# Kernel optimization log

Measured on AMD Instinct MI355X. Metric: run time of the kernel, lower is better.

## Reference

```python
import jax, jax.numpy as jnp
import numpy as np

# dims: B=batch, N1=in_channels (primary caps), P=pcap_n_dims, N2=n_caps, D=n_dims
B, N1, P, N2, D = 64, 1152, 8, 128, 16
ROUTINGS = 2


def squash(s, axis=-1):
    # squash_factor * unit_vector, with eps-stabilized norm (matches torch.finfo eps)
    sq_norm = jnp.sum(s * s, axis=axis, keepdims=True)
    norm = jnp.sqrt(sq_norm + jnp.finfo(s.dtype).eps)
    return (sq_norm / (1.0 + sq_norm)) * (s / norm)


def setup_inputs() -> dict:
    key = jax.random.key(0)
    k1, k2 = jax.random.split(key)
    x = jax.random.normal(k1, (B, N1, P), dtype=jnp.float32)
    # learned transform W: nn.Parameter(torch.randn(1, N1, N2, D, P)); leading 1 dropped
    W = jax.random.normal(k2, (N1, N2, D, P), dtype=jnp.float32)
    return {"x": x, "W": W}


def reference(x, W):
    b, n1 = x.shape[0], x.shape[1]
    n2 = W.shape[1]
    # caps2_predicted[b,i,n,d] = sum_p W[i,n,d,p] * x[b,i,p]  (the tiled batched matmul)
    pred = jnp.einsum('indp,bip->bind', W, x)  # [B, N1, N2, D]
    raw = jnp.zeros((b, n1, n2), dtype=pred.dtype)  # routing logits
    v = None
    for i in range(ROUTINGS):
        c = jax.nn.softmax(raw, axis=2)                  # softmax over output capsules
        s = jnp.einsum('bin,bind->bnd', c, pred)         # weighted sum over input caps
        v = squash(s, axis=-1)                           # [B, N2, D]
        if i < ROUTINGS - 1:
            # agreement: <prediction, output> over the D dimension
            raw = raw + jnp.einsum('bind,bnd->bin', pred, v)
    return v  # [B, n_caps, n_dims]
```

## Files before the change

### kernel.cpp

```cpp
#include <hip/hip_runtime.h>
#include <math.h>

#define B_   64
#define P_   8
#define N1_  1152
#define N2_  128
#define D_   16

#define NSPLIT 32
#define CHUNK  (N1_ / NSPLIT)
#define NIB    (CHUNK / 4)

typedef __attribute__((ext_vector_type(8)))  short bf16x8;
typedef __attribute__((ext_vector_type(4)))  float f32x4;
typedef __attribute__((ext_vector_type(16))) float f32x16;

__device__ inline void split_frag(float4 a0, float4 a1, bf16x8& hi, bf16x8& lo)
{
    float w[8] = {a0.x, a0.y, a0.z, a0.w, a1.x, a1.y, a1.z, a1.w};
#pragma unroll
    for (int j = 0; j < 8; ++j) {
        unsigned ub = __float_as_uint(w[j]);
        hi[j] = (short)(ub >> 16);
        float hif = __uint_as_float(ub & 0xffff0000u);
        float r = w[j] - hif;
        lo[j] = (short)(__float_as_uint(r) >> 16);
    }
}

__device__ inline void split_arr(const float* w, bf16x8& hi, bf16x8& lo)
{
#pragma unroll
    for (int j = 0; j < 8; ++j) {
        unsigned ub = __float_as_uint(w[j]);
        hi[j] = (short)(ub >> 16);
        float hif = __uint_as_float(ub & 0xffff0000u);
        float r = w[j] - hif;
        lo[j] = (short)(__float_as_uint(r) >> 16);
    }
}

__device__ inline void split4_pack(float4 s, uint2& hp, uint2& lp)
{
    float w[4] = {s.x, s.y, s.z, s.w};
    unsigned hs[4], ls[4];
#pragma unroll
    for (int j = 0; j < 4; ++j) {
        unsigned ub = __float_as_uint(w[j]);
        hs[j] = ub >> 16;
        float hif = __uint_as_float(ub & 0xffff0000u);
        float r = w[j] - hif;
        ls[j] = __float_as_uint(r) >> 16;
    }
    hp.x = hs[0] | (hs[1] << 16); hp.y = hs[2] | (hs[3] << 16);
    lp.x = ls[0] | (ls[1] << 16); lp.y = ls[2] | (ls[3] << 16);
}

__global__ __launch_bounds__(128) void k0_xt(const float* __restrict__ x,
                                             float* __restrict__ xt,
                                             unsigned short* __restrict__ xth,
                                             unsigned short* __restrict__ xtl,
                                             float* __restrict__ denom)
{
    const int i  = blockIdx.x;
    const int t  = threadIdx.x;
    const int b  = t >> 1, ph = t & 1;
    float4 v = *(const float4*)(x + ((size_t)b * N1_ + i) * P_ + ph * 4);
    const size_t off = (size_t)i * (64 * P_) + b * P_ + ph * 4;
    *(float4*)(xt + off) = v;
    uint2 hp, lp;
    split4_pack(v, hp, lp);
    *(uint2*)(xth + off) = hp;
    *(uint2*)(xtl + off) = lp;
    int z = i * 128 + t;
    if (z < N1_ * 64) denom[z] = 0.f;
}

__global__ __launch_bounds__(256) void k1_s0_mfma(const unsigned short* __restrict__ xth,
                                                  const unsigned short* __restrict__ xtl,
                                                  const float* __restrict__ W,
                                                  float* __restrict__ s0p)
{
    const int tid   = threadIdx.x;
    const int lane  = tid & 63;
    const int wv    = tid >> 6;
    const int col   = lane & 15;
    const int quad  = lane >> 4;
    const int b     = wv * 16 + col;
    const int nbase = blockIdx.x * 4;
    const int isp   = blockIdx.y;
    const int ibase = isp * CHUNK;

    f32x4 acc[4];
#pragma unroll
    for (int nn = 0; nn < 4; ++nn) acc[nn] = (f32x4){0.f, 0.f, 0.f, 0.f};

    const unsigned short* xh = xth + (size_t)(ibase + quad) * (64 * P_) + b * P_;
    const unsigned short* xl = xtl + (size_t)(ibase + quad) * (64 * P_) + b * P_;

    for (int ib = 0; ib < NIB; ++ib) {
        const int i0 = ibase + ib * 4;
        bf16x8 bhi = *(const bf16x8*)xh;
        bf16x8 blo = *(const bf16x8*)xl;
        xh += 4 * 64 * P_;
        xl += 4 * 64 * P_;
#pragma unroll
        for (int nn = 0; nn < 4; ++nn) {
            const float* wp = W + (((size_t)(i0 + quad) * N2_ + nbase + nn) * D_ + col) * P_;
            float4 wa = *(const float4*)wp;
            float4 wb = *(const float4*)(wp + 4);
            bf16x8 ahi, alo;
            split_frag(wa, wb, ahi, alo);
            acc[nn] = __builtin_amdgcn_mfma_f32_16x16x32_bf16(ahi, bhi, acc[nn], 0, 0, 0);
            acc[nn] = __builtin_amdgcn_mfma_f32_16x16x32_bf16(ahi, blo, acc[nn], 0, 0, 0);
            acc[nn] = __builtin_amdgcn_mfma_f32_16x16x32_bf16(alo, bhi, acc[nn], 0, 0, 0);
        }
    }
#pragma unroll
    for (int nn = 0; nn < 4; ++nn) {
        float4 v = make_float4(acc[nn][0], acc[nn][1], acc[nn][2], acc[nn][3]);
        *(float4*)(s0p + (size_t)isp * (B_ * N2_ * D_) + (size_t)b * (N2_ * D_)
                   + (nbase + nn) * D_ + quad * 4) = v;
    }
}

__global__ __launch_bounds__(256) void k2_squash(const float* __restrict__ spart,
                                                 float* __restrict__ vout,
                                                 unsigned short* __restrict__ v0h,
                                                 unsigned short* __restrict__ v0l,
                                                 float scale, int nsplit)
{
    int idx = blockIdx.x * 256 + threadIdx.x;
    float4 s = make_float4(0.f, 0.f, 0.f, 0.f);
    for (int sp = 0; sp < nsplit; ++sp) {
        float4 t = *(const float4*)(spart + (size_t)sp * (B_ * N2_ * D_) + (size_t)idx * 4);
        s.x += t.x; s.y += t.y; s.z += t.z; s.w += t.w;
    }
    s.x *= scale; s.y *= scale; s.z *= scale; s.w *= scale;
    float sq = s.x * s.x + s.y * s.y + s.z * s.z + s.w * s.w;
    sq += __shfl_xor(sq, 1);
    sq += __shfl_xor(sq, 2);
    float norm = sqrtf(sq + 1.1920929e-7f);
    float f = (sq / (1.f + sq)) / norm;
    float4 o = make_float4(s.x * f, s.y * f, s.z * f, s.w * f);
    *(float4*)(vout + (size_t)idx * 4) = o;
    if (v0h) {
        uint2 hp, lp;
        split4_pack(o, hp, lp);
        *(uint2*)(v0h + (size_t)idx * 4) = hp;
        *(uint2*)(v0l + (size_t)idx * 4) = lp;
    }
}

__global__ __launch_bounds__(256) void k3a2_mfma32(const float* __restrict__ xt,
                                                   const float* __restrict__ W,
                                                   const unsigned short* __restrict__ v0h,
                                                   const unsigned short* __restrict__ v0l,
                                                   float* __restrict__ e_t,
                                                   float* __restrict__ denom)
{
    const int tid  = threadIdx.x;
    const int lane = tid & 63;
    const int wv   = tid >> 6;
    const int m    = lane & 31;
    const int kh   = lane >> 5;
    const int isub = m >> 3;
    const int p    = m & 7;
    const int i0   = blockIdx.y * 4;
    const int nbase = blockIdx.x * 32 + wv * 8;

    float4 xq0[4], xq1[4];
#pragma unroll
    for (int is = 0; is < 4; ++is) {
        const float* xp = xt + (size_t)(i0 + is) * (64 * P_) + m * 8 + kh * 4;
        xq0[is] = *(const float4*)xp;
        xq1[is] = *(const float4*)(xp + 256);
    }

    float dacc[4] = {0.f, 0.f, 0.f, 0.f};

#pragma unroll 1
    for (int nt = 0; nt < 8; ++nt) {
        const int n = nbase + nt;

        bf16x8 vhi[2], vlo[2];
#pragma unroll
        for (int bt = 0; bt < 2; ++bt) {
            const size_t vo = (size_t)(bt * 32 + m) * (N2_ * D_) + n * D_ + kh * 8;
            vhi[bt] = *(const bf16x8*)(v0h + vo);
            vlo[bt] = *(const bf16x8*)(v0l + vo);
        }

        const float* wp = W + ((size_t)(i0 + isub) * N2_ + n) * (D_ * P_) + kh * 64 + p;
        float a[8];
#pragma unroll
        for (int j = 0; j < 8; ++j) a[j] = wp[8 * j];
        bf16x8 ahi, alo;
        split_arr(a, ahi, alo);

        f32x16 acc0, acc1;
#pragma unroll
        for (int r = 0; r < 16; ++r) { acc0[r] = 0.f; acc1[r] = 0.f; }
        acc0 = __builtin_amdgcn_mfma_f32_32x32x16_bf16(ahi, vhi[0], acc0, 0, 0, 0);
        acc0 = __builtin_amdgcn_mfma_f32_32x32x16_bf16(ahi, vlo[0], acc0, 0, 0, 0);
        acc0 = __builtin_amdgcn_mfma_f32_32x32x16_bf16(alo, vhi[0], acc0, 0, 0, 0);
        acc1 = __builtin_amdgcn_mfma_f32_32x32x16_bf16(ahi, vhi[1], acc1, 0, 0, 0);
        acc1 = __builtin_amdgcn_mfma_f32_32x32x16_bf16(ahi, vlo[1], acc1, 0, 0, 0);
        acc1 = __builtin_amdgcn_mfma_f32_32x32x16_bf16(alo, vhi[1], acc1, 0, 0, 0);

#pragma unroll
        for (int is = 0; is < 4; ++is) {
            float r0 = acc0[4 * is] * xq0[is].x + acc0[4 * is + 1] * xq0[is].y
                     + acc0[4 * is + 2] * xq0[is].z + acc0[4 * is + 3] * xq0[is].w;
            float r1 = acc1[4 * is] * xq1[is].x + acc1[4 * is + 1] * xq1[is].y
                     + acc1[4 * is + 2] * xq1[is].z + acc1[4 * is + 3] * xq1[is].w;
            r0 += __shfl_xor(r0, 32);
            r1 += __shfl_xor(r1, 32);
            float e = __expf(kh ? r1 : r0);
            e_t[(size_t)(i0 + is) * (N2_ * 64) + n * 64 + kh * 32 + m] = e;
            dacc[is] += e;
        }
    }

    __shared__ float dred[4][4][64];
#pragma unroll
    for (int is = 0; is < 4; ++is) dred[wv][is][kh * 32 + m] = dacc[is];
    __syncthreads();
    {
        const int is = tid >> 6;
        const int b  = tid & 63;
        float s = dred[0][is][b] + dred[1][is][b] + dred[2][is][b] + dred[3][is][b];
        atomicAdd(&denom[(size_t)(i0 + is) * 64 + b], s);
    }
}

__global__ __launch_bounds__(256) void k3c_s1_mfma(const float* __restrict__ xt,
                                                   const float* __restrict__ W,
                                                   const float* __restrict__ e_t,
                                                   const float* __restrict__ denom,
                                                   float* __restrict__ s1p)
{
    const int tid   = threadIdx.x;
    const int lane  = tid & 63;
    const int wv    = tid >> 6;
    const int col   = lane & 15;
    const int quad  = lane >> 4;
    const int n     = blockIdx.x * 4 + wv;
    const int isp   = blockIdx.y;
    const int ibase = isp * CHUNK;

    f32x4 acc[4];
#pragma unroll
    for (int bt = 0; bt < 4; ++bt) acc[bt] = (f32x4){0.f, 0.f, 0.f, 0.f};

    for (int ib = 0; ib < NIB; ++ib) {
        const int iq = ibase + ib * 4 + quad;
        const float* wp = W + ((size_t)iq * N2_ + n) * (D_ * P_) + col * P_;
        float4 wa = *(const float4*)wp;
        float4 wb = *(const float4*)(wp + 4);
        bf16x8 ahi, alo;
        split_frag(wa, wb, ahi, alo);
#pragma unroll
        for (int bt = 0; bt < 4; ++bt) {
            const int b = bt * 16 + col;
            const float* xp = xt + (size_t)iq * (64 * P_) + b * P_;
            float4 xa = *(const float4*)xp;
            float4 xb = *(const float4*)(xp + 4);
            float e  = e_t[((size_t)iq * N2_ + n) * 64 + b];
            float dv = denom[(size_t)iq * 64 + b];
            float c  = e * __builtin_amdgcn_rcpf(dv);
            float4 ya = make_float4(xa.x * c, xa.y * c, xa.z * c, xa.w * c);
            float4 yb = make_float4(xb.x * c, xb.y * c, xb.z * c, xb.w * c);
            bf16x8 bhi, blo;
            split_frag(ya, yb, bhi, blo);
            acc[bt] = __builtin_amdgcn_mfma_f32_16x16x32_bf16(ahi, bhi, acc[bt], 0, 0, 0);
            acc[bt] = __builtin_amdgcn_mfma_f32_16x16x32_bf16(ahi, blo, acc[bt], 0, 0, 0);
            acc[bt] = __builtin_amdgcn_mfma_f32_16x16x32_bf16(alo, bhi, acc[bt], 0, 0, 0);
        }
    }
#pragma unroll
    for (int bt = 0; bt < 4; ++bt) {
        const int b = bt * 16 + col;
        float4 v = make_float4(acc[bt][0], acc[bt][1], acc[bt][2], acc[bt][3]);
        *(float4*)(s1p + (size_t)isp * (B_ * N2_ * D_) + (size_t)b * (N2_ * D_)
                   + n * D_ + quad * 4) = v;
    }
}

extern "C" void kernel_launch(void* const* d_in, const int* in_sizes, int n_in,
                              void* d_out, int out_size, void* d_ws, size_t ws_size,
                              hipStream_t stream)
{
    const float* x = (const float*)d_in[0];
    const float* W = (const float*)d_in[1];
    float* out = (float*)d_out;

    float* s_part = (float*)d_ws;
    float* v0     = s_part + (size_t)NSPLIT * B_ * N2_ * D_;
    float* e_t    = v0 + B_ * N2_ * D_;
    float* xt     = e_t + (size_t)N1_ * N2_ * 64;
    float* denom  = xt + (size_t)N1_ * 64 * P_;
    unsigned short* xth = (unsigned short*)(denom + (size_t)N1_ * 64);
    unsigned short* xtl = xth + (size_t)N1_ * 64 * P_;
    unsigned short* v0h = xtl + (size_t)N1_ * 64 * P_;
    unsigned short* v0l = v0h + (size_t)B_ * N2_ * D_;

    k0_xt       <<<N1_,               128, 0, stream>>>(x, xt, xth, xtl, denom);
    k1_s0_mfma  <<<dim3(32, NSPLIT),  256, 0, stream>>>(xth, xtl, W, s_part);
    k2_squash   <<<128,               256, 0, stream>>>(s_part, v0, v0h, v0l, 1.f / 128.f, NSPLIT);
    k3a2_mfma32 <<<dim3(4, N1_ / 4),  256, 0, stream>>>(xt, W, v0h, v0l, e_t, denom);
    k3c_s1_mfma <<<dim3(32, NSPLIT),  256, 0, stream>>>(xt, W, e_t, denom, s_part);
    k2_squash   <<<128,               256, 0, stream>>>(s_part, out, nullptr, nullptr, 1.f, NSPLIT);
}
```

Measured before the change: 200.9 us.

## Remap s0 MFMA kernel so each wave owns one capsule across all batches

The first-routing-pass kernel now assigns each wave one output capsule n and loops over four batch tiles. Before, each wave covered one batch tile and four capsules, so the four waves of a block loaded and split the same W fragments four times. Now each W fragment is loaded and split into bf16 hi/lo once per wave, and the small x fragments are reloaded per batch tile instead. The split count over input capsules drops from 32 to 16, which halves the partial-sum buffer the squash kernel must reduce but also halves grid parallelism.

```diff
diff --git a/kernel.cpp b/kernel.cpp
--- a/kernel.cpp
+++ b/kernel.cpp
@@ -7,7 +7,7 @@
 #define N2_  128
 #define D_   16
 
-#define NSPLIT 32
+#define NSPLIT 16
 #define CHUNK  (N1_ / NSPLIT)
 #define NIB    (CHUNK / 4)
 
@@ -86,41 +86,38 @@
     const int wv    = tid >> 6;
     const int col   = lane & 15;
     const int quad  = lane >> 4;
-    const int b     = wv * 16 + col;
-    const int nbase = blockIdx.x * 4;
+    const int n     = blockIdx.x * 4 + wv;
     const int isp   = blockIdx.y;
     const int ibase = isp * CHUNK;
 
     f32x4 acc[4];
 #pragma unroll
-    for (int nn = 0; nn < 4; ++nn) acc[nn] = (f32x4){0.f, 0.f, 0.f, 0.f};
-
-    const unsigned short* xh = xth + (size_t)(ibase + quad) * (64 * P_) + b * P_;
-    const unsigned short* xl = xtl + (size_t)(ibase + quad) * (64 * P_) + b * P_;
+    for (int bt = 0; bt < 4; ++bt) acc[bt] = (f32x4){0.f, 0.f, 0.f, 0.f};
 
     for (int ib = 0; ib < NIB; ++ib) {
-        const int i0 = ibase + ib * 4;
-        bf16x8 bhi = *(const bf16x8*)xh;
-        bf16x8 blo = *(const bf16x8*)xl;
-        xh += 4 * 64 * P_;
-        xl += 4 * 64 * P_;
-#pragma unroll
-        for (int nn = 0; nn < 4; ++nn) {
-            const float* wp = W + (((size_t)(i0 + quad) * N2_ + nbase + nn) * D_ + col) * P_;
-            float4 wa = *(const float4*)wp;
-            float4 wb = *(const float4*)(wp + 4);
-            bf16x8 ahi, alo;
-            split_frag(wa, wb, ahi, alo);
-            acc[nn] = __builtin_amdgcn_mfma_f32_16x16x32_bf16(ahi, bhi, acc[nn], 0, 0, 0);
-            acc[nn] = __builtin_amdgcn_mfma_f32_16x16x32_bf16(ahi, blo, acc[nn], 0, 0, 0);
-            acc[nn] = __builtin_amdgcn_mfma_f32_16x16x32_bf16(alo, bhi, acc[nn], 0, 0, 0);
+        const int iq = ibase + ib * 4 + quad;
+        const float* wp = W + ((size_t)iq * N2_ + n) * (D_ * P_) + col * P_;
+        float4 wa = *(const float4*)wp;
+        float4 wb = *(const float4*)(wp + 4);
+        bf16x8 ahi, alo;
+        split_frag(wa, wb, ahi, alo);
+#pragma unroll
+        for (int bt = 0; bt < 4; ++bt) {
+            const int b = bt * 16 + col;
+            const size_t xo = (size_t)iq * (64 * P_) + b * P_;
+            bf16x8 bhi = *(const bf16x8*)(xth + xo);
+            bf16x8 blo = *(const bf16x8*)(xtl + xo);
+            acc[bt] = __builtin_amdgcn_mfma_f32_16x16x32_bf16(ahi, bhi, acc[bt], 0, 0, 0);
+            acc[bt] = __builtin_amdgcn_mfma_f32_16x16x32_bf16(ahi, blo, acc[bt], 0, 0, 0);
+            acc[bt] = __builtin_amdgcn_mfma_f32_16x16x32_bf16(alo, bhi, acc[bt], 0, 0, 0);
         }
     }
 #pragma unroll
-    for (int nn = 0; nn < 4; ++nn) {
-        float4 v = make_float4(acc[nn][0], acc[nn][1], acc[nn][2], acc[nn][3]);
+    for (int bt = 0; bt < 4; ++bt) {
+        const int b = bt * 16 + col;
+        float4 v = make_float4(acc[bt][0], acc[bt][1], acc[bt][2], acc[bt][3]);
         *(float4*)(s0p + (size_t)isp * (B_ * N2_ * D_) + (size_t)b * (N2_ * D_)
-                   + (nbase + nn) * D_ + quad * 4) = v;
+                   + n * D_ + quad * 4) = v;
     }
 }
 
```

Result: faster. 190.8 us (-5.0%).
